# Optimization experiments

Measured on AMD Instinct MI355X. Metric: run time of the kernel, lower is better.

## Reference

```python
import jax, jax.numpy as jnp
import numpy as np
from jax import lax

K = 3  # kernel size
PAD = K // 2


def _patches(x):
    # x: [B,C,H,W] -> [B,C,K*K,H,W] (zero-padded 'same' neighborhoods)
    B, C, H, W = x.shape
    xp = jnp.pad(x, ((0, 0), (0, 0), (PAD, PAD), (PAD, PAD)))
    ps = [xp[:, :, i:i + H, j:j + W] for i in range(K) for j in range(K)]
    return jnp.stack(ps, axis=2)


def pac_conv2d(x, guide, w, b):
    # Pixel-adaptive conv (pacnet, kernel_type='gaussian', not channel-wise).
    # adaptive kernel from guidance: exp(-0.5 * ||g_patch - g_center||^2)
    gp = _patches(guide)                      # [B,C,P,H,W]
    d2 = jnp.sum((gp - guide[:, :, None]) ** 2, axis=1)  # [B,P,H,W]
    kern = jnp.exp(-0.5 * d2)                 # [B,P,H,W]
    xp = _patches(x)                          # [B,Cin,P,H,W]
    wf = w.reshape(w.shape[0], w.shape[1], K * K)  # [Cout,Cin,P]
    out = jnp.einsum('bcphw,bphw,ocp->bohw', xp, kern, wf)
    return out + b[None, :, None, None]


def conv2d(x, w, b):
    out = lax.conv_general_dilated(x, w, (1, 1), 'SAME',
                                   dimension_numbers=('NCHW', 'OIHW', 'NCHW'))
    return out + b[None, :, None, None]


def setup_inputs() -> dict:
    key = jax.random.key(0)
    ks = jax.random.split(key, 10)
    B, C, H, W = 8, 64, 128, 128
    fan = C * K * K
    s = 1.0 / np.sqrt(fan)
    inp = {
        'x': jax.random.normal(ks[0], (B, C, H, W), jnp.float32),
        'edge': jax.random.normal(ks[1], (B, C, H, W), jnp.float32),
        'w_pac1': jax.random.normal(ks[2], (C, C, K, K), jnp.float32) * s,
        'b_pac1': jax.random.normal(ks[3], (C,), jnp.float32) * s,
        'w_pac2': jax.random.normal(ks[4], (C, C, K, K), jnp.float32) * s,
        'b_pac2': jax.random.normal(ks[5], (C,), jnp.float32) * s,
        'w_e1': jax.random.normal(ks[6], (C, C, K, K), jnp.float32) * s,
        'b_e1': jax.random.normal(ks[7], (C,), jnp.float32) * s,
        'w_e2': jax.random.normal(ks[8], (C, C, K, K), jnp.float32) * s,
        'b_e2': jax.random.normal(ks[9], (C,), jnp.float32) * s,
    }
    return inp


def reference(x, edge, w_pac1, b_pac1, w_pac2, b_pac2, w_e1, b_e1, w_e2, b_e2):
    res_scale = 1.0
    # i=0: pac conv on sr (guided by current edge), plain conv on edge
    res_sr = pac_conv2d(x, edge, w_pac1, b_pac1)
    res_edge = conv2d(edge, w_e1, b_e1)
    # i=1: activation on both
    res_sr = jax.nn.relu(res_sr)
    res_edge = jax.nn.relu(res_edge)
    # i=2: pac conv guided by updated edge, plain conv on edge
    res_sr = pac_conv2d(res_sr, res_edge, w_pac2, b_pac2)
    res_edge = conv2d(res_edge, w_e2, b_e2)
    # dual residual
    res_sr = x + res_sr * res_scale
    res_edge = edge + res_edge * res_scale
    return (res_sr, res_edge)
```

## Files before the change

kernel.cpp:

```cpp
#include <hip/hip_runtime.h>

typedef unsigned short u16;
typedef __attribute__((ext_vector_type(8))) short s8;
typedef __attribute__((ext_vector_type(4))) float f4;

#define B_  8
#define C_  64
#define H_  128
#define W_  128
#define HW_ (H_*W_)
#define PITCH 72
#define WSZ 36864

static __device__ __forceinline__ u16 f2bu(float f) {
    union { float f; unsigned u; } c; c.f = f;
    unsigned u = c.u;
    u += 0x7fffu + ((u >> 16) & 1u);
    return (u16)(u >> 16);
}
static __device__ __forceinline__ float bu2f(u16 u) {
    union { unsigned u; float f; } c; c.u = ((unsigned)u) << 16; return c.f;
}

__global__ __launch_bounds__(256) void transpose2(
    const float* __restrict__ x, const float* __restrict__ edge,
    u16* __restrict__ x_t, u16* __restrict__ edge_t)
{
    __shared__ float s[16][68];
    const int t  = threadIdx.x;
    const int h  = blockIdx.x >> 3;
    const int w0 = (blockIdx.x & 7) * 16;
    const int b  = blockIdx.y;
    const float* src = blockIdx.z ? edge : x;
    u16* dst = blockIdx.z ? edge_t : x_t;
    {
        int c = t >> 2, wq = t & 3;
        float4 v = *(const float4*)(src + ((size_t)b*C_ + c)*HW_ + h*W_ + w0 + wq*4);
        s[wq*4+0][c] = v.x; s[wq*4+1][c] = v.y; s[wq*4+2][c] = v.z; s[wq*4+3][c] = v.w;
    }
    __syncthreads();
    {
        int w = t >> 4, cg = t & 15;
        float4 v = *(const float4*)(&s[w][cg*4]);
        ushort4 o; o.x = f2bu(v.x); o.y = f2bu(v.y); o.z = f2bu(v.z); o.w = f2bu(v.w);
        *(ushort4*)(dst + ((size_t)b*HW_ + h*W_ + w0 + w)*64 + cg*4) = o;
    }
}

__global__ __launch_bounds__(256) void wt_all(
    const float* __restrict__ w0, const float* __restrict__ w1,
    const float* __restrict__ w2, const float* __restrict__ w3,
    u16* __restrict__ dst)
{
    int idx = blockIdx.x*256 + threadIdx.x;
    int cid = blockIdx.y;
    const float* w = (cid == 0) ? w0 : (cid == 1) ? w1 : (cid == 2) ? w2 : w3;
    int p = idx >> 12, o = (idx >> 6) & 63, c = idx & 63;
    dst[(size_t)cid*WSZ + idx] = f2bu(w[((size_t)o*64 + c)*9 + p]);
}

static __device__ __forceinline__ void stage_tile(
    u16* __restrict__ s_t, const u16* __restrict__ src, int b, int th0, int tw0, int t)
{
    for (int i = t; i < 18*18*8; i += 256) {
        int pix = i >> 3, ch = i & 7;
        int rr = pix / 18, ww = pix - rr*18;
        int gr = th0 + rr - 1, gw = tw0 + ww - 1;
        uint4 v = {0u,0u,0u,0u};
        if ((unsigned)gr < (unsigned)H_ && (unsigned)gw < (unsigned)W_)
            v = *(const uint4*)(src + ((size_t)b*HW_ + gr*W_ + gw)*64 + ch*8);
        *(uint4*)(&s_t[pix*PITCH + ch*8]) = v;
    }
}

template<bool PAC>
static __device__ __forceinline__ void conv_core(
    const u16* __restrict__ s_t, const float* __restrict__ s_k,
    const u16* __restrict__ w, const float* __restrict__ bias,
    f4 acc[4][4], int wv, int ln, int quad)
{
#pragma unroll
    for (int mf = 0; mf < 4; ++mf) {
        f4 bv;
#pragma unroll
        for (int r = 0; r < 4; ++r) bv[r] = bias[mf*16 + quad*4 + r];
#pragma unroll
        for (int nf = 0; nf < 4; ++nf) acc[mf][nf] = bv;
    }

#pragma unroll
    for (int p = 0; p < 9; ++p) {
        const int dr = p / 3, dc = p - dr*3;
        s8 a[4][2];
#pragma unroll
        for (int mf = 0; mf < 4; ++mf)
#pragma unroll
            for (int kc = 0; kc < 2; ++kc)
                a[mf][kc] = *(const s8*)(w + (((size_t)p*64 + mf*16 + ln)*64 + kc*32 + quad*8));
        s8 bfr[4][2];
#pragma unroll
        for (int nf = 0; nf < 4; ++nf) {
            const u16* base = &s_t[((wv*4 + nf + dr)*18 + ln + dc)*PITCH];
#pragma unroll
            for (int kc = 0; kc < 2; ++kc)
                bfr[nf][kc] = *(const s8*)(base + kc*32 + quad*8);
        }
        if (PAC) {
            float kv[4];
#pragma unroll
            for (int nf = 0; nf < 4; ++nf)
                kv[nf] = s_k[p*256 + (wv*4 + nf)*16 + ln];
#pragma unroll
            for (int mf = 0; mf < 4; ++mf)
#pragma unroll
                for (int nf = 0; nf < 4; ++nf) {
                    f4 d = {0.f, 0.f, 0.f, 0.f};
                    d = __builtin_amdgcn_mfma_f32_16x16x32_bf16(a[mf][0], bfr[nf][0], d, 0, 0, 0);
                    d = __builtin_amdgcn_mfma_f32_16x16x32_bf16(a[mf][1], bfr[nf][1], d, 0, 0, 0);
                    acc[mf][nf] += kv[nf] * d;
                }
        } else {
#pragma unroll
            for (int mf = 0; mf < 4; ++mf)
#pragma unroll
                for (int nf = 0; nf < 4; ++nf) {
                    acc[mf][nf] = __builtin_amdgcn_mfma_f32_16x16x32_bf16(a[mf][0], bfr[nf][0], acc[mf][nf], 0, 0, 0);
                    acc[mf][nf] = __builtin_amdgcn_mfma_f32_16x16x32_bf16(a[mf][1], bfr[nf][1], acc[mf][nf], 0, 0, 0);
                }
        }
    }
}

static __device__ __forceinline__ void store_t(
    u16* __restrict__ out, f4 acc[4][4], int b, int th0, int tw0, int wv, int ln, int quad)
{
#pragma unroll
    for (int mf = 0; mf < 4; ++mf)
#pragma unroll
        for (int nf = 0; nf < 4; ++nf) {
            f4 v = acc[mf][nf];
            ushort4 o;
            o.x = f2bu(fmaxf(v[0], 0.f)); o.y = f2bu(fmaxf(v[1], 0.f));
            o.z = f2bu(fmaxf(v[2], 0.f)); o.w = f2bu(fmaxf(v[3], 0.f));
            size_t pix = (size_t)b*HW_ + (th0 + wv*4 + nf)*W_ + tw0 + ln;
            *(ushort4*)(out + pix*64 + mf*16 + quad*4) = o;
        }
}

static __device__ __forceinline__ void store_f(
    float* __restrict__ out, const u16* __restrict__ resid_t,
    f4 acc[4][4], int b, int th0, int tw0, int wv, int ln, int quad)
{
#pragma unroll
    for (int mf = 0; mf < 4; ++mf)
#pragma unroll
        for (int nf = 0; nf < 4; ++nf) {
            size_t pix = (size_t)b*HW_ + (th0 + wv*4 + nf)*W_ + tw0 + ln;
            ushort4 rv = *(const ushort4*)(resid_t + pix*64 + mf*16 + quad*4);
            float rr[4] = {bu2f(rv.x), bu2f(rv.y), bu2f(rv.z), bu2f(rv.w)};
#pragma unroll
            for (int r = 0; r < 4; ++r) {
                int och = mf*16 + quad*4 + r;
                out[((size_t)b*C_ + och)*HW_ + (th0 + wv*4 + nf)*W_ + tw0 + ln]
                    = acc[mf][nf][r] + rr[r];
            }
        }
}

template<bool STAGE1>
__global__ __launch_bounds__(256, 2) void fused_stage(
    const u16* __restrict__ inA_t, const u16* __restrict__ inB_t,
    const u16* __restrict__ wA, const u16* __restrict__ wB,
    const float* __restrict__ biasA, const float* __restrict__ biasB,
    const u16* __restrict__ residA_t, const u16* __restrict__ residB_t,
    u16* __restrict__ outA_t, u16* __restrict__ outB_t,
    float* __restrict__ outA_f, float* __restrict__ outB_f)
{
    __shared__ u16   s_t[18*18*PITCH];
    __shared__ float s_k[9*16*16];

    const int t    = threadIdx.x;
    const int b    = blockIdx.y;
    const int th0  = (blockIdx.x >> 3) * 16;
    const int tw0  = (blockIdx.x & 7) * 16;
    const int wv   = t >> 6;
    const int lane = t & 63;
    const int ln   = lane & 15;
    const int quad = lane >> 4;

    stage_tile(s_t, inA_t, b, th0, tw0, t);
    __syncthreads();

    {
        const int px = t & 15, py = t >> 4;
        float d2[9];
#pragma unroll
        for (int p = 0; p < 9; ++p) d2[p] = 0.f;
        const u16* cb = &s_t[((py+1)*18 + (px+1))*PITCH];
#pragma unroll 1
        for (int co = 0; co < 8; ++co) {
            s8 c8 = *(const s8*)(cb + co*8);
            float cf[8];
#pragma unroll
            for (int j = 0; j < 8; ++j) cf[j] = bu2f((u16)c8[j]);
#pragma unroll
            for (int p = 0; p < 9; ++p) {
                s8 n8 = *(const s8*)(&s_t[((py + p/3)*18 + px + p%3)*PITCH + co*8]);
#pragma unroll
                for (int j = 0; j < 8; ++j) {
                    float d = bu2f((u16)n8[j]) - cf[j];
                    d2[p] += d * d;
                }
            }
        }
#pragma unroll
        for (int p = 0; p < 9; ++p)
            s_k[p*256 + py*16 + px] = __expf(-0.5f * d2[p]);
    }

    {
        f4 acc[4][4];
        conv_core<false>(s_t, nullptr, wA, biasA, acc, wv, ln, quad);
        if (STAGE1) store_t(outA_t, acc, b, th0, tw0, wv, ln, quad);
        else        store_f(outA_f, residA_t, acc, b, th0, tw0, wv, ln, quad);
    }

    __syncthreads();
    stage_tile(s_t, inB_t, b, th0, tw0, t);
    __syncthreads();

    {
        f4 acc[4][4];
        conv_core<true>(s_t, s_k, wB, biasB, acc, wv, ln, quad);
        if (STAGE1) store_t(outB_t, acc, b, th0, tw0, wv, ln, quad);
        else        store_f(outB_f, residB_t, acc, b, th0, tw0, wv, ln, quad);
    }
}

extern "C" void kernel_launch(void* const* d_in, const int* in_sizes, int n_in,
                              void* d_out, int out_size, void* d_ws, size_t ws_size,
                              hipStream_t stream)
{
    const float* x      = (const float*)d_in[0];
    const float* edge   = (const float*)d_in[1];
    const float* w_pac1 = (const float*)d_in[2];
    const float* b_pac1 = (const float*)d_in[3];
    const float* w_pac2 = (const float*)d_in[4];
    const float* b_pac2 = (const float*)d_in[5];
    const float* w_e1   = (const float*)d_in[6];
    const float* b_e1   = (const float*)d_in[7];
    const float* w_e2   = (const float*)d_in[8];
    const float* b_e2   = (const float*)d_in[9];

    float* out_sr   = (float*)d_out;
    float* out_edge = out_sr + (size_t)B_*C_*HW_;

    const size_t NT = (size_t)B_*HW_*64;
    u16* x_t         = (u16*)d_ws;
    u16* edge_t      = x_t + NT;
    u16* res_edge1_t = edge_t + NT;
    u16* res_sr1_t   = res_edge1_t + NT;
    u16* w_t         = res_sr1_t + NT;

    dim3 blk(256);

    transpose2<<<dim3(H_*8, B_, 2), blk, 0, stream>>>(x, edge, x_t, edge_t);
    wt_all<<<dim3(144, 4), blk, 0, stream>>>(w_e1, w_pac1, w_e2, w_pac2, w_t);

    fused_stage<true ><<<dim3(64, B_), blk, 0, stream>>>(
        edge_t, x_t, w_t + 0*WSZ, w_t + 1*WSZ, b_e1, b_pac1,
        nullptr, nullptr, res_edge1_t, res_sr1_t, nullptr, nullptr);
    fused_stage<false><<<dim3(64, B_), blk, 0, stream>>>(
        res_edge1_t, res_sr1_t, w_t + 2*WSZ, w_t + 3*WSZ, b_e2, b_pac2,
        edge_t, x_t, nullptr, nullptr, out_edge, out_sr);
}
```

Baseline: 264.4 us.

## Halve spatial tile and split waves over channels and rows for occupancy

Shrinks each block's tile from 16x16 to 8x16 pixels and splits the four waves into a 2x2 grid over output channels and pixel rows, halving per-wave accumulators. The Gaussian kernel computation is split across two thread halves by neighbor index. Launch bounds rise to 4 blocks per CU and the grid doubles, aiming to improve occupancy and latency hiding. The trade-off is higher halo overhead and less weight-fragment reuse per wave.

```diff
diff --git a/kernel.cpp b/kernel.cpp
--- a/kernel.cpp
+++ b/kernel.cpp
@@ -12,6 +12,7 @@
 #define PITCH 72
 #define WSZ 36864
 
+
 static __device__ __forceinline__ u16 f2bu(float f) {
     union { float f; unsigned u; } c; c.f = f;
     unsigned u = c.u;
@@ -62,7 +63,7 @@
 static __device__ __forceinline__ void stage_tile(
     u16* __restrict__ s_t, const u16* __restrict__ src, int b, int th0, int tw0, int t)
 {
-    for (int i = t; i < 18*18*8; i += 256) {
+    for (int i = t; i < 10*18*8; i += 256) {
         int pix = i >> 3, ch = i & 7;
         int rr = pix / 18, ww = pix - rr*18;
         int gr = th0 + rr - 1, gw = tw0 + ww - 1;
@@ -77,13 +78,13 @@
 static __device__ __forceinline__ void conv_core(
     const u16* __restrict__ s_t, const float* __restrict__ s_k,
     const u16* __restrict__ w, const float* __restrict__ bias,
-    f4 acc[4][4], int wv, int ln, int quad)
-{
-#pragma unroll
-    for (int mf = 0; mf < 4; ++mf) {
+    f4 acc[2][4], int wvM, int wvN, int ln, int quad)
+{
+#pragma unroll
+    for (int mf = 0; mf < 2; ++mf) {
         f4 bv;
 #pragma unroll
-        for (int r = 0; r < 4; ++r) bv[r] = bias[mf*16 + quad*4 + r];
+        for (int r = 0; r < 4; ++r) bv[r] = bias[wvM*32 + mf*16 + quad*4 + r];
 #pragma unroll
         for (int nf = 0; nf < 4; ++nf) acc[mf][nf] = bv;
     }
@@ -91,16 +92,16 @@
 #pragma unroll
     for (int p = 0; p < 9; ++p) {
         const int dr = p / 3, dc = p - dr*3;
-        s8 a[4][2];
-#pragma unroll
-        for (int mf = 0; mf < 4; ++mf)
+        s8 a[2][2];
+#pragma unroll
+        for (int mf = 0; mf < 2; ++mf)
 #pragma unroll
             for (int kc = 0; kc < 2; ++kc)
-                a[mf][kc] = *(const s8*)(w + (((size_t)p*64 + mf*16 + ln)*64 + kc*32 + quad*8));
+                a[mf][kc] = *(const s8*)(w + (((size_t)p*64 + wvM*32 + mf*16 + ln)*64 + kc*32 + quad*8));
         s8 bfr[4][2];
 #pragma unroll
         for (int nf = 0; nf < 4; ++nf) {
-            const u16* base = &s_t[((wv*4 + nf + dr)*18 + ln + dc)*PITCH];
+            const u16* base = &s_t[((wvN*4 + nf + dr)*18 + ln + dc)*PITCH];
 #pragma unroll
             for (int kc = 0; kc < 2; ++kc)
                 bfr[nf][kc] = *(const s8*)(base + kc*32 + quad*8);
@@ -109,9 +110,9 @@
             float kv[4];
 #pragma unroll
             for (int nf = 0; nf < 4; ++nf)
-                kv[nf] = s_k[p*256 + (wv*4 + nf)*16 + ln];
-#pragma unroll
-            for (int mf = 0; mf < 4; ++mf)
+                kv[nf] = s_k[p*128 + (wvN*4 + nf)*16 + ln];
+#pragma unroll
+            for (int mf = 0; mf < 2; ++mf)
 #pragma unroll
                 for (int nf = 0; nf < 4; ++nf) {
                     f4 d = {0.f, 0.f, 0.f, 0.f};
@@ -121,7 +122,7 @@
                 }
         } else {
 #pragma unroll
-            for (int mf = 0; mf < 4; ++mf)
+            for (int mf = 0; mf < 2; ++mf)
 #pragma unroll
                 for (int nf = 0; nf < 4; ++nf) {
                     acc[mf][nf] = __builtin_amdgcn_mfma_f32_16x16x32_bf16(a[mf][0], bfr[nf][0], acc[mf][nf], 0, 0, 0);
@@ -132,43 +133,44 @@
 }
 
 static __device__ __forceinline__ void store_t(
-    u16* __restrict__ out, f4 acc[4][4], int b, int th0, int tw0, int wv, int ln, int quad)
-{
-#pragma unroll
-    for (int mf = 0; mf < 4; ++mf)
+    u16* __restrict__ out, f4 acc[2][4], int b, int th0, int tw0,
+    int wvM, int wvN, int ln, int quad)
+{
+#pragma unroll
+    for (int mf = 0; mf < 2; ++mf)
 #pragma unroll
         for (int nf = 0; nf < 4; ++nf) {
             f4 v = acc[mf][nf];
             ushort4 o;
             o.x = f2bu(fmaxf(v[0], 0.f)); o.y = f2bu(fmaxf(v[1], 0.f));
             o.z = f2bu(fmaxf(v[2], 0.f)); o.w = f2bu(fmaxf(v[3], 0.f));
-            size_t pix = (size_t)b*HW_ + (th0 + wv*4 + nf)*W_ + tw0 + ln;
-            *(ushort4*)(out + pix*64 + mf*16 + quad*4) = o;
+            size_t pix = (size_t)b*HW_ + (th0 + wvN*4 + nf)*W_ + tw0 + ln;
+            *(ushort4*)(out + pix*64 + wvM*32 + mf*16 + quad*4) = o;
         }
 }
 
 static __device__ __forceinline__ void store_f(
     float* __restrict__ out, const u16* __restrict__ resid_t,
-    f4 acc[4][4], int b, int th0, int tw0, int wv, int ln, int quad)
-{
-#pragma unroll
-    for (int mf = 0; mf < 4; ++mf)
+    f4 acc[2][4], int b, int th0, int tw0, int wvM, int wvN, int ln, int quad)
+{
+#pragma unroll
+    for (int mf = 0; mf < 2; ++mf)
 #pragma unroll
         for (int nf = 0; nf < 4; ++nf) {
-            size_t pix = (size_t)b*HW_ + (th0 + wv*4 + nf)*W_ + tw0 + ln;
-            ushort4 rv = *(const ushort4*)(resid_t + pix*64 + mf*16 + quad*4);
+            size_t pix = (size_t)b*HW_ + (th0 + wvN*4 + nf)*W_ + tw0 + ln;
+            ushort4 rv = *(const ushort4*)(resid_t + pix*64 + wvM*32 + mf*16 + quad*4);
             float rr[4] = {bu2f(rv.x), bu2f(rv.y), bu2f(rv.z), bu2f(rv.w)};
 #pragma unroll
             for (int r = 0; r < 4; ++r) {
-                int och = mf*16 + quad*4 + r;
-                out[((size_t)b*C_ + och)*HW_ + (th0 + wv*4 + nf)*W_ + tw0 + ln]
+                int och = wvM*32 + mf*16 + quad*4 + r;
+                out[((size_t)b*C_ + och)*HW_ + (th0 + wvN*4 + nf)*W_ + tw0 + ln]
                     = acc[mf][nf][r] + rr[r];
             }
         }
 }
 
 template<bool STAGE1>
-__global__ __launch_bounds__(256, 2) void fused_stage(
+__global__ __launch_bounds__(256, 4) void fused_stage(
     const u16* __restrict__ inA_t, const u16* __restrict__ inB_t,
     const u16* __restrict__ wA, const u16* __restrict__ wB,
     const float* __restrict__ biasA, const float* __restrict__ biasB,
@@ -176,14 +178,16 @@
     u16* __restrict__ outA_t, u16* __restrict__ outB_t,
     float* __restrict__ outA_f, float* __restrict__ outB_f)
 {
-    __shared__ u16   s_t[18*18*PITCH];
-    __shared__ float s_k[9*16*16];
+    __shared__ u16   s_t[10*18*PITCH];
+    __shared__ float s_k[9*128];
 
     const int t    = threadIdx.x;
     const int b    = blockIdx.y;
-    const int th0  = (blockIdx.x >> 3) * 16;
+    const int th0  = (blockIdx.x >> 3) * 8;
     const int tw0  = (blockIdx.x & 7) * 16;
     const int wv   = t >> 6;
+    const int wvM  = wv >> 1;
+    const int wvN  = wv & 1;
     const int lane = t & 63;
     const int ln   = lane & 15;
     const int quad = lane >> 4;
@@ -192,11 +196,15 @@
     __syncthreads();
 
     {
-        const int px = t & 15, py = t >> 4;
-        float d2[9];
-#pragma unroll
-        for (int p = 0; p < 9; ++p) d2[p] = 0.f;
-        const u16* cb = &s_t[((py+1)*18 + (px+1))*PITCH];
+        const int px   = t & 127;
+        const int half = t >> 7;
+        const int p0   = half ? 5 : 0;
+        const int np   = half ? 4 : 5;
+        const int py   = px >> 4, pxc = px & 15;
+        float d2[5];
+#pragma unroll
+        for (int k = 0; k < 5; ++k) d2[k] = 0.f;
+        const u16* cb = &s_t[((py+1)*18 + (pxc+1))*PITCH];
 #pragma unroll 1
         for (int co = 0; co < 8; ++co) {
             s8 c8 = *(const s8*)(cb + co*8);
@@ -204,25 +212,29 @@
 #pragma unroll
             for (int j = 0; j < 8; ++j) cf[j] = bu2f((u16)c8[j]);
 #pragma unroll
-            for (int p = 0; p < 9; ++p) {
-                s8 n8 = *(const s8*)(&s_t[((py + p/3)*18 + px + p%3)*PITCH + co*8]);
-#pragma unroll
-                for (int j = 0; j < 8; ++j) {
-                    float d = bu2f((u16)n8[j]) - cf[j];
-                    d2[p] += d * d;
+            for (int k = 0; k < 5; ++k) {
+                if (k < np) {
+                    int p = p0 + k;
+                    int dr = p / 3, dc = p - dr*3;
+                    s8 n8 = *(const s8*)(&s_t[((py + dr)*18 + pxc + dc)*PITCH + co*8]);
+#pragma unroll
+                    for (int j = 0; j < 8; ++j) {
+                        float d = bu2f((u16)n8[j]) - cf[j];
+                        d2[k] += d * d;
+                    }
                 }
             }
         }
 #pragma unroll
-        for (int p = 0; p < 9; ++p)
-            s_k[p*256 + py*16 + px] = __expf(-0.5f * d2[p]);
-    }
-
-    {
-        f4 acc[4][4];
-        conv_core<false>(s_t, nullptr, wA, biasA, acc, wv, ln, quad);
-        if (STAGE1) store_t(outA_t, acc, b, th0, tw0, wv, ln, quad);
-        else        store_f(outA_f, residA_t, acc, b, th0, tw0, wv, ln, quad);
+        for (int k = 0; k < 5; ++k)
+            if (k < np) s_k[(p0+k)*128 + px] = __expf(-0.5f * d2[k]);
+    }
+
+    {
+        f4 acc[2][4];
+        conv_core<false>(s_t, nullptr, wA, biasA, acc, wvM, wvN, ln, quad);
+        if (STAGE1) store_t(outA_t, acc, b, th0, tw0, wvM, wvN, ln, quad);
+        else        store_f(outA_f, residA_t, acc, b, th0, tw0, wvM, wvN, ln, quad);
     }
 
     __syncthreads();
@@ -230,10 +242,10 @@
     __syncthreads();
 
     {
-        f4 acc[4][4];
-        conv_core<true>(s_t, s_k, wB, biasB, acc, wv, ln, quad);
-        if (STAGE1) store_t(outB_t, acc, b, th0, tw0, wv, ln, quad);
-        else        store_f(outB_f, residB_t, acc, b, th0, tw0, wv, ln, quad);
+        f4 acc[2][4];
+        conv_core<true>(s_t, s_k, wB, biasB, acc, wvM, wvN, ln, quad);
+        if (STAGE1) store_t(outB_t, acc, b, th0, tw0, wvM, wvN, ln, quad);
+        else        store_f(outB_f, residB_t, acc, b, th0, tw0, wvM, wvN, ln, quad);
     }
 }
 
@@ -267,10 +279,10 @@
     transpose2<<<dim3(H_*8, B_, 2), blk, 0, stream>>>(x, edge, x_t, edge_t);
     wt_all<<<dim3(144, 4), blk, 0, stream>>>(w_e1, w_pac1, w_e2, w_pac2, w_t);
 
-    fused_stage<true ><<<dim3(64, B_), blk, 0, stream>>>(
+    fused_stage<true ><<<dim3(128, B_), blk, 0, stream>>>(
         edge_t, x_t, w_t + 0*WSZ, w_t + 1*WSZ, b_e1, b_pac1,
         nullptr, nullptr, res_edge1_t, res_sr1_t, nullptr, nullptr);
-    fused_stage<false><<<dim3(64, B_), blk, 0, stream>>>(
+    fused_stage<false><<<dim3(128, B_), blk, 0, stream>>>(
         res_edge1_t, res_sr1_t, w_t + 2*WSZ, w_t + 3*WSZ, b_e2, b_pac2,
         edge_t, x_t, nullptr, nullptr, out_edge, out_sr);
 }
```

Measured after the change: 339.3 us. +28.3%, slower.
